# Optimization experiments

Measured on AMD Instinct MI355X. Metric: run time of the kernel, lower is better.

## Reference

```python
import jax, jax.numpy as jnp
import numpy as np

MU = 136.72353790613718
SIGMA = 62.34640414043511


def setup_inputs() -> dict:
    key = jax.random.key(0)
    k1, k2, k3, k4 = jax.random.split(key, 4)
    B, D = 16384, 2048
    return {
        "minibatch_features": jax.random.normal(k1, (B, D), dtype=jnp.float32),
        "label": jax.random.normal(k2, (B,), dtype=jnp.float32),
        "idx1": jax.random.randint(k3, (B,), 0, B),
        "idx2": jax.random.randint(k4, (B,), 0, B),
    }


def _fix_indices(idx1, idx2, B):
    # Deterministically map raw random ints to valid (a, b) with a != i, b != i, b != a,
    # mirroring random.sample's constraints plus the while-loop check in the original.
    i = jnp.arange(B)
    a = (i + 1 + idx1 % (B - 1)) % B            # a != i
    b = (i + 1 + idx2 % (B - 1)) % B            # b != i
    b = jnp.where(b == a, (i + 1 + (idx2 + 1) % (B - 1)) % B, b)  # b != a, still != i
    return i, a, b


def reference(minibatch_features, label, idx1, idx2):
    feats = minibatch_features
    B = feats.shape[0]
    i_arr, a, b = _fix_indices(idx1, idx2, B)

    def step(lab, xs):
        i, i1, i2 = xs
        anchor = feats[i]                        # [D]
        t1, t2 = feats[i1], feats[i2]
        # nn.L1Loss(reduction='sum') on scalars == abs diff.
        # NOTE: lab may contain already-normalized entries for indices < i (original mutates label in place).
        ld1 = jnp.abs(lab[i] - lab[i1])
        ld2 = jnp.abs(lab[i] - lab[i2])
        cond = ld1 >= ld2
        near = jnp.where(cond, t2, t1)
        far = jnp.where(cond, t1, t2)
        near_l = jnp.where(cond, lab[i2], lab[i1])
        far_l = jnp.where(cond, lab[i1], lab[i2])
        li = (lab[i] - MU) / SIGMA
        lab = lab.at[i].set(li)                  # in-place mutation replicated
        nl = (near_l - MU) / SIGMA
        fl = (far_l - MU) / SIGMA
        dp = jnp.sum((anchor - near) ** 2)
        dn = jnp.sum((anchor - far) ** 2)
        alpha = (li - fl) ** 2 - (li - nl) ** 2
        loss = jax.nn.relu(dp - dn + 0.5 * alpha)  # margin=0.5 hardcoded in TripletLoss_self
        return lab, loss

    _, losses = jax.lax.scan(step, label, (i_arr, a, b))
    # `if loss >= 0` is always true after relu, so the sum is unconditional.
    return jnp.sum(losses)
```

## Files before the change

### kernel.cpp

```cpp
#include <hip/hip_runtime.h>

#define MU_F    136.72353790613718f
#define SIGMA_F 62.34640414043511f

__global__ __launch_bounds__(256) void triplet_per_row(
    const float* __restrict__ feats,
    const float* __restrict__ label,
    const int*   __restrict__ idx1,
    const int*   __restrict__ idx2,
    float* __restrict__ ws,
    int B, int D)
{
    const int j = blockIdx.x;

    const int r1 = idx1[j] % (B - 1);
    int aIdx = j + 1 + r1; if (aIdx >= B) aIdx -= B;
    const int r2 = idx2[j] % (B - 1);
    int bIdx = j + 1 + r2; if (bIdx >= B) bIdx -= B;
    if (bIdx == aIdx) {
        const int r2b = (idx2[j] + 1) % (B - 1);
        bIdx = j + 1 + r2b; if (bIdx >= B) bIdx -= B;
    }

    const float lj = label[j];
    float la = label[aIdx]; if (aIdx < j) la = (la - MU_F) / SIGMA_F;
    float lb = label[bIdx]; if (bIdx < j) lb = (lb - MU_F) / SIGMA_F;

    const float* __restrict__ fj = feats + (size_t)j    * (size_t)D;
    const float* __restrict__ fa = feats + (size_t)aIdx * (size_t)D;
    const float* __restrict__ fb = feats + (size_t)bIdx * (size_t)D;

    float pa = 0.f, pb = 0.f;
    const int t = threadIdx.x;
    for (int k = t * 8; k < D; k += 256 * 8) {
        const float4 x0 = *(const float4*)(fj + k);
        const float4 x1 = *(const float4*)(fj + k + 4);
        const float4 a0 = *(const float4*)(fa + k);
        const float4 a1 = *(const float4*)(fa + k + 4);
        const float4 b0 = *(const float4*)(fb + k);
        const float4 b1 = *(const float4*)(fb + k + 4);
        float d;
        d = x0.x - a0.x; pa += d * d;   d = x0.y - a0.y; pa += d * d;
        d = x0.z - a0.z; pa += d * d;   d = x0.w - a0.w; pa += d * d;
        d = x1.x - a1.x; pa += d * d;   d = x1.y - a1.y; pa += d * d;
        d = x1.z - a1.z; pa += d * d;   d = x1.w - a1.w; pa += d * d;
        d = x0.x - b0.x; pb += d * d;   d = x0.y - b0.y; pb += d * d;
        d = x0.z - b0.z; pb += d * d;   d = x0.w - b0.w; pb += d * d;
        d = x1.x - b1.x; pb += d * d;   d = x1.y - b1.y; pb += d * d;
        d = x1.z - b1.z; pb += d * d;   d = x1.w - b1.w; pb += d * d;
    }

    #pragma unroll
    for (int off = 32; off > 0; off >>= 1) {
        pa += __shfl_down(pa, off);
        pb += __shfl_down(pb, off);
    }
    __shared__ float sa[4], sb[4];
    const int wid = t >> 6, lane = t & 63;
    if (lane == 0) { sa[wid] = pa; sb[wid] = pb; }
    __syncthreads();

    if (t == 0) {
        const float da = sa[0] + sa[1] + sa[2] + sa[3];
        const float db = sb[0] + sb[1] + sb[2] + sb[3];

        const float ld1 = fabsf(lj - la);
        const float ld2 = fabsf(lj - lb);
        const bool cond = (ld1 >= ld2);

        const float near_l = cond ? lb : la;
        const float far_l  = cond ? la : lb;
        const float dp     = cond ? db : da;
        const float dn     = cond ? da : db;

        const float li = (lj     - MU_F) / SIGMA_F;
        const float nl = (near_l - MU_F) / SIGMA_F;
        const float fl = (far_l  - MU_F) / SIGMA_F;

        const float alpha = (li - fl) * (li - fl) - (li - nl) * (li - nl);
        const float loss  = dp - dn + 0.5f * alpha;
        ws[j] = loss > 0.f ? loss : 0.f;
    }
}

__global__ __launch_bounds__(256) void reduce_losses(
    const float* __restrict__ ws, float* __restrict__ out, int n)
{
    float s = 0.f;
    for (int k = threadIdx.x; k < n; k += 256) s += ws[k];
    #pragma unroll
    for (int off = 32; off > 0; off >>= 1) s += __shfl_down(s, off);
    __shared__ float sm[4];
    const int wid = threadIdx.x >> 6, lane = threadIdx.x & 63;
    if (lane == 0) sm[wid] = s;
    __syncthreads();
    if (threadIdx.x == 0) out[0] = sm[0] + sm[1] + sm[2] + sm[3];
}

extern "C" void kernel_launch(void* const* d_in, const int* in_sizes, int n_in,
                              void* d_out, int out_size, void* d_ws, size_t ws_size,
                              hipStream_t stream)
{
    const float* feats = (const float*)d_in[0];
    const float* label = (const float*)d_in[1];
    const int*   idx1  = (const int*)d_in[2];
    const int*   idx2  = (const int*)d_in[3];

    const int B = in_sizes[1];
    const int D = in_sizes[0] / B;

    float* ws = (float*)d_ws;

    triplet_per_row<<<B, 256, 0, stream>>>(feats, label, idx1, idx2, ws, B, D);
    reduce_losses<<<1, 256, 0, stream>>>(ws, (float*)d_out, B);
}
```

Before: 76.28 us.

## Map one wavefront per row and vectorize the final loss reduction

Each 64-lane wavefront now handles one anchor row instead of a 256-thread block, so each block processes four rows and the shared-memory cross-wave reduction and __syncthreads are removed. Each lane strides over the row with float4 loads and a 4x unroll, giving 8 iterations per lane for D=2048. The final reduction kernel reads float4 chunks. The vectorized reduce assumes n is a multiple of 4 and that ws is 16-byte aligned.

```diff
diff --git a/kernel.cpp b/kernel.cpp
--- a/kernel.cpp
+++ b/kernel.cpp
@@ -3,7 +3,7 @@
 #define MU_F    136.72353790613718f
 #define SIGMA_F 62.34640414043511f
 
-__global__ __launch_bounds__(256) void triplet_per_row(
+__global__ __launch_bounds__(256) void triplet_wave_per_row(
     const float* __restrict__ feats,
     const float* __restrict__ label,
     const int*   __restrict__ idx1,
@@ -11,7 +11,10 @@
     float* __restrict__ ws,
     int B, int D)
 {
-    const int j = blockIdx.x;
+    const int wid  = threadIdx.x >> 6;
+    const int lane = threadIdx.x & 63;
+    const int j    = blockIdx.x * 4 + wid;
+    if (j >= B) return;
 
     const int r1 = idx1[j] % (B - 1);
     int aIdx = j + 1 + r1; if (aIdx >= B) aIdx -= B;
@@ -31,23 +34,16 @@
     const float* __restrict__ fb = feats + (size_t)bIdx * (size_t)D;
 
     float pa = 0.f, pb = 0.f;
-    const int t = threadIdx.x;
-    for (int k = t * 8; k < D; k += 256 * 8) {
-        const float4 x0 = *(const float4*)(fj + k);
-        const float4 x1 = *(const float4*)(fj + k + 4);
-        const float4 a0 = *(const float4*)(fa + k);
-        const float4 a1 = *(const float4*)(fa + k + 4);
-        const float4 b0 = *(const float4*)(fb + k);
-        const float4 b1 = *(const float4*)(fb + k + 4);
+    #pragma unroll 4
+    for (int k = lane * 4; k < D; k += 64 * 4) {
+        const float4 x = *(const float4*)(fj + k);
+        const float4 a = *(const float4*)(fa + k);
+        const float4 b = *(const float4*)(fb + k);
         float d;
-        d = x0.x - a0.x; pa += d * d;   d = x0.y - a0.y; pa += d * d;
-        d = x0.z - a0.z; pa += d * d;   d = x0.w - a0.w; pa += d * d;
-        d = x1.x - a1.x; pa += d * d;   d = x1.y - a1.y; pa += d * d;
-        d = x1.z - a1.z; pa += d * d;   d = x1.w - a1.w; pa += d * d;
-        d = x0.x - b0.x; pb += d * d;   d = x0.y - b0.y; pb += d * d;
-        d = x0.z - b0.z; pb += d * d;   d = x0.w - b0.w; pb += d * d;
-        d = x1.x - b1.x; pb += d * d;   d = x1.y - b1.y; pb += d * d;
-        d = x1.z - b1.z; pb += d * d;   d = x1.w - b1.w; pb += d * d;
+        d = x.x - a.x; pa += d * d;   d = x.y - a.y; pa += d * d;
+        d = x.z - a.z; pa += d * d;   d = x.w - a.w; pa += d * d;
+        d = x.x - b.x; pb += d * d;   d = x.y - b.y; pb += d * d;
+        d = x.z - b.z; pb += d * d;   d = x.w - b.w; pb += d * d;
     }
 
     #pragma unroll
@@ -55,14 +51,9 @@
         pa += __shfl_down(pa, off);
         pb += __shfl_down(pb, off);
     }
-    __shared__ float sa[4], sb[4];
-    const int wid = t >> 6, lane = t & 63;
-    if (lane == 0) { sa[wid] = pa; sb[wid] = pb; }
-    __syncthreads();
 
-    if (t == 0) {
-        const float da = sa[0] + sa[1] + sa[2] + sa[3];
-        const float db = sb[0] + sb[1] + sb[2] + sb[3];
+    if (lane == 0) {
+        const float da = pa, db = pb;
 
         const float ld1 = fabsf(lj - la);
         const float ld2 = fabsf(lj - lb);
@@ -87,7 +78,10 @@
     const float* __restrict__ ws, float* __restrict__ out, int n)
 {
     float s = 0.f;
-    for (int k = threadIdx.x; k < n; k += 256) s += ws[k];
+    for (int k = threadIdx.x * 4; k < n; k += 256 * 4) {
+        const float4 v = *(const float4*)(ws + k);
+        s += (v.x + v.y) + (v.z + v.w);
+    }
     #pragma unroll
     for (int off = 32; off > 0; off >>= 1) s += __shfl_down(s, off);
     __shared__ float sm[4];
@@ -111,6 +105,6 @@
 
     float* ws = (float*)d_ws;
 
-    triplet_per_row<<<B, 256, 0, stream>>>(feats, label, idx1, idx2, ws, B, D);
+    triplet_wave_per_row<<<(B + 3) / 4, 256, 0, stream>>>(feats, label, idx1, idx2, ws, B, D);
     reduce_losses<<<1, 256, 0, stream>>>(ws, (float*)d_out, B);
 }
```

Measured after the change: 65.89 us. -13.6%, faster.
